# Performance work log

Measured on AMD Instinct MI355X. Metric: run time of the kernel, lower is better.

The kernel has to match this reference:

```python
import jax, jax.numpy as jnp
import numpy as np

# Dim order: [N, K, C, P, Q, R, S]; memory levels: [L0_Registers, L1_Accumulator, L2_Scratchpad, L3_DRAM]
# Tensor types: 0=Input(N,C,P,Q) 1=Weight(K,C,R,S) 2=Output(N,K,P,Q)
DIM_MASK = jnp.array([[1,0,1,1,1,0,0],
                      [0,1,1,0,0,1,1],
                      [1,1,0,1,1,0,0]], dtype=bool)
# reuse dims: Input->K, Weight->N,P,Q, Output->C,R,S
REUSE_MASK = jnp.array([[0,1,0,0,0,0,0],
                        [1,0,0,1,1,0,0],
                        [0,0,1,0,0,1,1]], dtype=bool)

BYTES = 4.0
CLK_MHZ = 1000.0
DRAM_BW_GB_S = 100.0
PE_MAC_EPA_PJ = 0.56
L0_REG_EPA_PJ = 0.18
L1_BASE_EPA_PJ = 0.52
L1_COEFF_PJ_KB = 0.01
L2_BASE_EPA_PJ = 1.2
L2_COEFF_PJ_KB = 0.002
AREA_PER_PE = 0.01
AREA_PER_KB = 0.005

G = 500000  # number of (unfused) layers / fusion groups


def setup_inputs() -> dict:
    key = jax.random.key(0)
    k1, k2 = jax.random.split(key)
    temporal = 1.0 + jax.random.uniform(k1, (G, 7, 4), dtype=jnp.float32)
    spatial = 1.0 + jax.random.uniform(k2, (G, 7, 4), dtype=jnp.float32)
    return {
        "temporal_factors": temporal,
        "spatial_factors": spatial,
        "num_pes": jnp.array([256.0], dtype=jnp.float32),
        "buffer_sizes_kb": jnp.array([1.0, 64.0, 512.0], dtype=jnp.float32),  # L0, L1, L2
    }


def _masked_prod(x, mask):
    # x: [G,7,L], mask: [3,7] -> [G,3,L] product over masked dims
    return jnp.prod(jnp.where(mask[None, :, :, None], x[:, None, :, :], 1.0), axis=2)


def reference(temporal_factors, spatial_factors, num_pes, buffer_sizes_kb):
    pe = num_pes[0]
    sq = jnp.sqrt(pe)

    cumTS = jnp.cumprod(temporal_factors * spatial_factors, axis=2)  # prefix prod over levels
    cumT = jnp.cumprod(temporal_factors, axis=2)
    sufT = jnp.flip(jnp.cumprod(jnp.flip(temporal_factors, 2), 2), 2)  # suffix prod over levels

    macs = jnp.prod(cumTS[:, :, -1], axis=1)  # [G] product of full dim sizes

    fp = _masked_prod(cumTS, DIM_MASK)      # [G,3,4] data footprint up to level l
    outer = _masked_prod(sufT, DIM_MASK)    # [G,3,4] outer iterations from level l up
    ru = _masked_prod(cumT, REUSE_MASK)     # [G,3,4] reuse factor up to level l

    # interfaces (upper->lower): L3->L2, L2->L1, L1->L0
    low = jnp.array([2, 1, 0])
    up = jnp.array([3, 2, 1])
    acc = (fp[:, :, low] * (outer[:, :, up] / (ru[:, :, low] + 1e-9)) * BYTES).sum(axis=1)  # [G,3]

    # latency
    onchip_bw = 2.0 * sq * BYTES * CLK_MHZ * 1e6 / 1e9
    bw = jnp.stack([jnp.full((), DRAM_BW_GB_S), onchip_bw, onchip_bw])  # upper level bw per interface
    mem_lat = acc / (bw[None, :] * 1e9 + 1e-9)
    comp_lat = macs / (pe * CLK_MHZ * 1e6 + 1e-9)
    total_latency = jnp.maximum(comp_lat, mem_lat.max(axis=1)).sum()

    # energy (per interface, keyed by lower level: L2, L1, L0)
    epa = jnp.stack([
        L2_BASE_EPA_PJ + L2_COEFF_PJ_KB * buffer_sizes_kb[2],
        L1_BASE_EPA_PJ + L1_COEFF_PJ_KB * (buffer_sizes_kb[1] / sq),
        jnp.full((), L0_REG_EPA_PJ),
    ])
    total_energy = (macs * PE_MAC_EPA_PJ).sum() + ((acc / 4.0) @ epa).sum()

    # buffer mismatch for buffer levels L0, L1, L2
    req_kb = fp[:, :, :3].sum(axis=1) * BYTES / 1024.0  # [G,3]
    deficit = jax.nn.relu(req_kb - buffer_sizes_kb[None, :])
    total_mismatch = (deficit ** 2).sum()

    area = pe * AREA_PER_PE + (buffer_sizes_kb * AREA_PER_KB).sum()
    return (total_latency, total_energy, area, total_mismatch)
```

## Files before the change

### kernel.cpp

```cpp
#include <hip/hip_runtime.h>
#include <hip/hip_bf16.h>


typedef const __attribute__((address_space(1))) void* gptr_t;
typedef __attribute__((address_space(3))) void* lptr_t;

#define BLK   256
#define NBK   256
#define WPB   4
#define NWAVE (NBK * WPB)
#define TGRP  64

__device__ __forceinline__ float fast_rcp(float x) {
    float r;
    asm("v_rcp_f32 %0, %1" : "=v"(r) : "v"(x));
    return r;
}

__global__ __launch_bounds__(BLK) void hpm_main(
    const float* __restrict__ T, const float* __restrict__ S,
    const float* __restrict__ PE, const float* __restrict__ BUF,
    double* __restrict__ part, int G)
{
    __shared__ float lds[WPB][2][2][TGRP * 28];

    const int tid  = threadIdx.x;
    const int w    = tid >> 6;
    const int lane = tid & 63;
    const int W    = blockIdx.x * WPB + w;
    const int NT   = G / TGRP;
    const int cnt  = (NT > W) ? ((NT - 1 - W) / NWAVE + 1) : 0;

    const float pe = PE[0];
    const float sq = sqrtf(pe);
    const float b0 = BUF[0], b1 = BUF[1], b2 = BUF[2];
    const float inv_bw_dram   = 1.0f / (100.0f * 1e9f + 1e-9f);
    const float inv_bw_onchip = 1.0f / (sq * 8e9f + 1e-9f);
    const float epa0 = 1.2f  + 0.002f * b2;
    const float epa1 = 0.52f + 0.01f  * (b1 / sq);
    const float epa2 = 0.18f;
    const float inv_pe = 1.0f / (pe * 1e9f + 1e-9f);
    asm volatile("s_waitcnt vmcnt(0) lgkmcnt(0)" ::: "memory");

    constexpr unsigned IN_D = 0x1D, WT_D = 0x66, OU_D = 0x1B;
    constexpr unsigned IN_R = 0x02, WT_R = 0x19, OU_R = 0x64;

    auto issue = [&](int t, int buf) {
        const float* gT = T + (size_t)t * (TGRP * 28);
        const float* gS = S + (size_t)t * (TGRP * 28);
        #pragma unroll
        for (int k = 0; k < 7; ++k) {
            const int fo = (k * 64 + lane) * 4;
            __builtin_amdgcn_global_load_lds((gptr_t)(gT + fo),
                                             (lptr_t)&lds[w][buf][0][k * 256], 16, 0, 0);
            __builtin_amdgcn_global_load_lds((gptr_t)(gS + fo),
                                             (lptr_t)&lds[w][buf][1][k * 256], 16, 0, 0);
        }
    };

    double latA = 0.0, enA = 0.0, misA = 0.0;

    auto accumulate = [&](const float4* tv, const float4* sv) {
        float fpI[3] = {1.f,1.f,1.f}, fpW[3] = {1.f,1.f,1.f}, fpO[3] = {1.f,1.f,1.f};
        float otI[3] = {1.f,1.f,1.f}, otW[3] = {1.f,1.f,1.f}, otO[3] = {1.f,1.f,1.f};
        float ruI[3] = {1.f,1.f,1.f}, ruW[3] = {1.f,1.f,1.f}, ruO[3] = {1.f,1.f,1.f};
        float macs = 1.f;

        #pragma unroll
        for (int d = 0; d < 7; ++d) {
            const float4 tt = tv[d];
            const float4 ss = sv[d];

            const float ct0 = tt.x;
            const float ct1 = ct0 * tt.y;
            const float ct2 = ct1 * tt.z;
            const float u0 = tt.x * ss.x, u1 = tt.y * ss.y;
            const float u2 = tt.z * ss.z, u3 = tt.w * ss.w;
            const float cs0 = u0;
            const float cs1 = cs0 * u1;
            const float cs2 = cs1 * u2;
            const float cs3 = cs2 * u3;
            const float st3 = tt.w;
            const float st2 = tt.z * st3;
            const float st1 = tt.y * st2;

            macs *= cs3;

            if ((IN_D >> d) & 1) {
                fpI[0] *= cs0; fpI[1] *= cs1; fpI[2] *= cs2;
                otI[0] *= st1; otI[1] *= st2; otI[2] *= st3;
            }
            if ((WT_D >> d) & 1) {
                fpW[0] *= cs0; fpW[1] *= cs1; fpW[2] *= cs2;
                otW[0] *= st1; otW[1] *= st2; otW[2] *= st3;
            }
            if ((OU_D >> d) & 1) {
                fpO[0] *= cs0; fpO[1] *= cs1; fpO[2] *= cs2;
                otO[0] *= st1; otO[1] *= st2; otO[2] *= st3;
            }
            if ((IN_R >> d) & 1) { ruI[0] *= ct0; ruI[1] *= ct1; ruI[2] *= ct2; }
            if ((WT_R >> d) & 1) { ruW[0] *= ct0; ruW[1] *= ct1; ruW[2] *= ct2; }
            if ((OU_R >> d) & 1) { ruO[0] *= ct0; ruO[1] *= ct1; ruO[2] *= ct2; }
        }

        const float acc0 = 4.f * ( fpI[2] * otI[2] * fast_rcp(ruI[2] + 1e-9f)
                                 + fpW[2] * otW[2] * fast_rcp(ruW[2] + 1e-9f)
                                 + fpO[2] * otO[2] * fast_rcp(ruO[2] + 1e-9f) );
        const float acc1 = 4.f * ( fpI[1] * otI[1] * fast_rcp(ruI[1] + 1e-9f)
                                 + fpW[1] * otW[1] * fast_rcp(ruW[1] + 1e-9f)
                                 + fpO[1] * otO[1] * fast_rcp(ruO[1] + 1e-9f) );
        const float acc2 = 4.f * ( fpI[0] * otI[0] * fast_rcp(ruI[0] + 1e-9f)
                                 + fpW[0] * otW[0] * fast_rcp(ruW[0] + 1e-9f)
                                 + fpO[0] * otO[0] * fast_rcp(ruO[0] + 1e-9f) );

        const float ml = fmaxf(acc0 * inv_bw_dram, fmaxf(acc1, acc2) * inv_bw_onchip);
        const float cl = macs * inv_pe;
        latA += (double)fmaxf(cl, ml);

        enA += (double)(macs * 0.56f + (acc0 * epa0 + acc1 * epa1 + acc2 * epa2) * 0.25f);

        const float c = 4.f / 1024.f;
        const float r0 = (fpI[0] + fpW[0] + fpO[0]) * c;
        const float r1 = (fpI[1] + fpW[1] + fpO[1]) * c;
        const float r2 = (fpI[2] + fpW[2] + fpO[2]) * c;
        const float d0 = fmaxf(r0 - b0, 0.f);
        const float d1 = fmaxf(r1 - b1, 0.f);
        const float d2 = fmaxf(r2 - b2, 0.f);
        misA += (double)d0 * d0 + (double)d1 * d1 + (double)d2 * d2;
    };

    if (cnt > 0) issue(W, 0);
    if (cnt > 1) issue(W + NWAVE, 1);

    for (int i = 0; i < cnt; ++i) {
        if (i + 1 < cnt) asm volatile("s_waitcnt vmcnt(14)" ::: "memory");
        else             asm volatile("s_waitcnt vmcnt(0)"  ::: "memory");

        const int buf = i & 1;
        float4 tv[7], sv[7];
        {
            const float4* Tl = reinterpret_cast<const float4*>(&lds[w][buf][0][lane * 28]);
            const float4* Sl = reinterpret_cast<const float4*>(&lds[w][buf][1][lane * 28]);
            #pragma unroll
            for (int d = 0; d < 7; ++d) { tv[d] = Tl[d]; sv[d] = Sl[d]; }
        }
        asm volatile("s_waitcnt lgkmcnt(0)" ::: "memory");
        __builtin_amdgcn_sched_barrier(0);

        if (i + 2 < cnt) issue(W + (i + 2) * NWAVE, buf);

        accumulate(tv, sv);
    }

    if (W == NWAVE - 1) {
        const int g = NT * TGRP + lane;
        if (g < G) {
            float4 tv[7], sv[7];
            const float4* Tp = reinterpret_cast<const float4*>(T) + (size_t)g * 7;
            const float4* Sp = reinterpret_cast<const float4*>(S) + (size_t)g * 7;
            #pragma unroll
            for (int d = 0; d < 7; ++d) { tv[d] = Tp[d]; sv[d] = Sp[d]; }
            accumulate(tv, sv);
        }
    }

    #pragma unroll
    for (int off = 32; off > 0; off >>= 1) {
        latA += __shfl_down(latA, off);
        enA  += __shfl_down(enA,  off);
        misA += __shfl_down(misA, off);
    }

    __shared__ double sred[3][WPB];
    if (lane == 0) { sred[0][w] = latA; sred[1][w] = enA; sred[2][w] = misA; }
    __syncthreads();

    if (tid == 0) {
        double L = 0.0, E = 0.0, M = 0.0;
        #pragma unroll
        for (int v = 0; v < WPB; ++v) { L += sred[0][v]; E += sred[1][v]; M += sred[2][v]; }
        part[0 * NBK + blockIdx.x] = L;
        part[1 * NBK + blockIdx.x] = E;
        part[2 * NBK + blockIdx.x] = M;
    }
}

__global__ __launch_bounds__(256) void hpm_final(
    const double* __restrict__ part,
    const float* __restrict__ PE, const float* __restrict__ BUF,
    float* __restrict__ out)
{
    const int tid = threadIdx.x;
    double L = 0.0, E = 0.0, M = 0.0;
    if (tid < NBK) {
        L = part[0 * NBK + tid];
        E = part[1 * NBK + tid];
        M = part[2 * NBK + tid];
    }

    #pragma unroll
    for (int off = 32; off > 0; off >>= 1) {
        L += __shfl_down(L, off);
        E += __shfl_down(E, off);
        M += __shfl_down(M, off);
    }

    __shared__ double sred[3][4];
    const int wid  = tid >> 6;
    const int lane = tid & 63;
    if (lane == 0) { sred[0][wid] = L; sred[1][wid] = E; sred[2][wid] = M; }
    __syncthreads();

    if (tid == 0) {
        double Lt = 0.0, Et = 0.0, Mt = 0.0;
        #pragma unroll
        for (int v = 0; v < 4; ++v) { Lt += sred[0][v]; Et += sred[1][v]; Mt += sred[2][v]; }
        out[0] = (float)Lt;
        out[1] = (float)Et;
        out[2] = PE[0] * 0.01f + (BUF[0] + BUF[1] + BUF[2]) * 0.005f;
        out[3] = (float)Mt;
    }
}

extern "C" void kernel_launch(void* const* d_in, const int* in_sizes, int n_in,
                              void* d_out, int out_size, void* d_ws, size_t ws_size,
                              hipStream_t stream) {
    const float* T   = (const float*)d_in[0];
    const float* S   = (const float*)d_in[1];
    const float* PE  = (const float*)d_in[2];
    const float* BUF = (const float*)d_in[3];
    float* out = (float*)d_out;
    double* ws = (double*)d_ws;

    const int G = in_sizes[0] / 28;

    hipLaunchKernelGGL(hpm_main, dim3(NBK), dim3(BLK), 0, stream,
                       T, S, PE, BUF, ws, G);
    hipLaunchKernelGGL(hpm_final, dim3(1), dim3(256), 0, stream,
                       ws, PE, BUF, out);
}
```

Baseline: 25.93 us.

## Replace persistent LDS-pipelined waves with one-thread-per-layer grid and direct loads

Drops the persistent 256-block kernel that double-buffered tiles through LDS with global_load_lds. Each thread now handles one layer, loading its 28 floats straight from global memory with float4 loads, and the grid grows to about 1954 blocks. The final kernel loops over the larger partial array. This removes the async-copy pipeline and its waitcnt management, but gives up the coalesced staging: each thread's 112-byte stride loads are less coalesced, and there are more partials to reduce.

Measured after the change: 27.18 us. 1.05x slower.

```diff
diff --git a/kernel.cpp b/kernel.cpp
--- a/kernel.cpp
+++ b/kernel.cpp
@@ -2,14 +2,7 @@
 #include <hip/hip_bf16.h>
 
 
-typedef const __attribute__((address_space(1))) void* gptr_t;
-typedef __attribute__((address_space(3))) void* lptr_t;
-
-#define BLK   256
-#define NBK   256
-#define WPB   4
-#define NWAVE (NBK * WPB)
-#define TGRP  64
+#define BLK 256
 
 __device__ __forceinline__ float fast_rcp(float x) {
     float r;
@@ -20,51 +13,39 @@
 __global__ __launch_bounds__(BLK) void hpm_main(
     const float* __restrict__ T, const float* __restrict__ S,
     const float* __restrict__ PE, const float* __restrict__ BUF,
-    double* __restrict__ part, int G)
+    double* __restrict__ part, int G, int NB)
 {
-    __shared__ float lds[WPB][2][2][TGRP * 28];
+    const int tid = threadIdx.x;
+    const int g   = blockIdx.x * BLK + tid;
 
-    const int tid  = threadIdx.x;
-    const int w    = tid >> 6;
-    const int lane = tid & 63;
-    const int W    = blockIdx.x * WPB + w;
-    const int NT   = G / TGRP;
-    const int cnt  = (NT > W) ? ((NT - 1 - W) / NWAVE + 1) : 0;
+    double lat = 0.0, en = 0.0, mis = 0.0;
 
-    const float pe = PE[0];
-    const float sq = sqrtf(pe);
-    const float b0 = BUF[0], b1 = BUF[1], b2 = BUF[2];
-    const float inv_bw_dram   = 1.0f / (100.0f * 1e9f + 1e-9f);
-    const float inv_bw_onchip = 1.0f / (sq * 8e9f + 1e-9f);
-    const float epa0 = 1.2f  + 0.002f * b2;
-    const float epa1 = 0.52f + 0.01f  * (b1 / sq);
-    const float epa2 = 0.18f;
-    const float inv_pe = 1.0f / (pe * 1e9f + 1e-9f);
-    asm volatile("s_waitcnt vmcnt(0) lgkmcnt(0)" ::: "memory");
+    if (g < G) {
+        float4 tv[7], sv[7];
+        const float4* Tp = reinterpret_cast<const float4*>(T) + (size_t)g * 7;
+        const float4* Sp = reinterpret_cast<const float4*>(S) + (size_t)g * 7;
+        #pragma unroll
+        for (int d = 0; d < 7; ++d) tv[d] = Tp[d];
+        #pragma unroll
+        for (int d = 0; d < 7; ++d) sv[d] = Sp[d];
 
-    constexpr unsigned IN_D = 0x1D, WT_D = 0x66, OU_D = 0x1B;
-    constexpr unsigned IN_R = 0x02, WT_R = 0x19, OU_R = 0x64;
+        const float pe = PE[0];
+        const float sq = sqrtf(pe);
+        const float b0 = BUF[0], b1 = BUF[1], b2 = BUF[2];
+        const float inv_bw_dram   = 1.0f / (100.0f * 1e9f + 1e-9f);
+        const float inv_bw_onchip = 1.0f / (sq * 8e9f + 1e-9f);
+        const float epa0 = 1.2f  + 0.002f * b2;
+        const float epa1 = 0.52f + 0.01f  * (b1 / sq);
+        const float epa2 = 0.18f;
+        const float inv_pe = 1.0f / (pe * 1e9f + 1e-9f);
 
-    auto issue = [&](int t, int buf) {
-        const float* gT = T + (size_t)t * (TGRP * 28);
-        const float* gS = S + (size_t)t * (TGRP * 28);
-        #pragma unroll
-        for (int k = 0; k < 7; ++k) {
-            const int fo = (k * 64 + lane) * 4;
-            __builtin_amdgcn_global_load_lds((gptr_t)(gT + fo),
-                                             (lptr_t)&lds[w][buf][0][k * 256], 16, 0, 0);
-            __builtin_amdgcn_global_load_lds((gptr_t)(gS + fo),
-                                             (lptr_t)&lds[w][buf][1][k * 256], 16, 0, 0);
-        }
-    };
-
-    double latA = 0.0, enA = 0.0, misA = 0.0;
-
-    auto accumulate = [&](const float4* tv, const float4* sv) {
         float fpI[3] = {1.f,1.f,1.f}, fpW[3] = {1.f,1.f,1.f}, fpO[3] = {1.f,1.f,1.f};
         float otI[3] = {1.f,1.f,1.f}, otW[3] = {1.f,1.f,1.f}, otO[3] = {1.f,1.f,1.f};
         float ruI[3] = {1.f,1.f,1.f}, ruW[3] = {1.f,1.f,1.f}, ruO[3] = {1.f,1.f,1.f};
         float macs = 1.f;
+
+        constexpr unsigned IN_D = 0x1D, WT_D = 0x66, OU_D = 0x1B;
+        constexpr unsigned IN_R = 0x02, WT_R = 0x19, OU_R = 0x64;
 
         #pragma unroll
         for (int d = 0; d < 7; ++d) {
@@ -115,9 +96,9 @@
 
         const float ml = fmaxf(acc0 * inv_bw_dram, fmaxf(acc1, acc2) * inv_bw_onchip);
         const float cl = macs * inv_pe;
-        latA += (double)fmaxf(cl, ml);
+        lat = (double)fmaxf(cl, ml);
 
-        enA += (double)(macs * 0.56f + (acc0 * epa0 + acc1 * epa1 + acc2 * epa2) * 0.25f);
+        en = (double)(macs * 0.56f + (acc0 * epa0 + acc1 * epa1 + acc2 * epa2) * 0.25f);
 
         const float c = 4.f / 1024.f;
         const float r0 = (fpI[0] + fpW[0] + fpO[0]) * c;
@@ -126,76 +107,43 @@
         const float d0 = fmaxf(r0 - b0, 0.f);
         const float d1 = fmaxf(r1 - b1, 0.f);
         const float d2 = fmaxf(r2 - b2, 0.f);
-        misA += (double)d0 * d0 + (double)d1 * d1 + (double)d2 * d2;
-    };
-
-    if (cnt > 0) issue(W, 0);
-    if (cnt > 1) issue(W + NWAVE, 1);
-
-    for (int i = 0; i < cnt; ++i) {
-        if (i + 1 < cnt) asm volatile("s_waitcnt vmcnt(14)" ::: "memory");
-        else             asm volatile("s_waitcnt vmcnt(0)"  ::: "memory");
-
-        const int buf = i & 1;
-        float4 tv[7], sv[7];
-        {
-            const float4* Tl = reinterpret_cast<const float4*>(&lds[w][buf][0][lane * 28]);
-            const float4* Sl = reinterpret_cast<const float4*>(&lds[w][buf][1][lane * 28]);
-            #pragma unroll
-            for (int d = 0; d < 7; ++d) { tv[d] = Tl[d]; sv[d] = Sl[d]; }
-        }
-        asm volatile("s_waitcnt lgkmcnt(0)" ::: "memory");
-        __builtin_amdgcn_sched_barrier(0);
-
-        if (i + 2 < cnt) issue(W + (i + 2) * NWAVE, buf);
-
-        accumulate(tv, sv);
-    }
-
-    if (W == NWAVE - 1) {
-        const int g = NT * TGRP + lane;
-        if (g < G) {
-            float4 tv[7], sv[7];
-            const float4* Tp = reinterpret_cast<const float4*>(T) + (size_t)g * 7;
-            const float4* Sp = reinterpret_cast<const float4*>(S) + (size_t)g * 7;
-            #pragma unroll
-            for (int d = 0; d < 7; ++d) { tv[d] = Tp[d]; sv[d] = Sp[d]; }
-            accumulate(tv, sv);
-        }
+        mis = (double)d0 * d0 + (double)d1 * d1 + (double)d2 * d2;
     }
 
     #pragma unroll
     for (int off = 32; off > 0; off >>= 1) {
-        latA += __shfl_down(latA, off);
-        enA  += __shfl_down(enA,  off);
-        misA += __shfl_down(misA, off);
+        lat += __shfl_down(lat, off);
+        en  += __shfl_down(en,  off);
+        mis += __shfl_down(mis, off);
     }
 
-    __shared__ double sred[3][WPB];
-    if (lane == 0) { sred[0][w] = latA; sred[1][w] = enA; sred[2][w] = misA; }
+    __shared__ double sred[3][4];
+    const int wid  = tid >> 6;
+    const int lane = tid & 63;
+    if (lane == 0) { sred[0][wid] = lat; sred[1][wid] = en; sred[2][wid] = mis; }
     __syncthreads();
 
     if (tid == 0) {
         double L = 0.0, E = 0.0, M = 0.0;
         #pragma unroll
-        for (int v = 0; v < WPB; ++v) { L += sred[0][v]; E += sred[1][v]; M += sred[2][v]; }
-        part[0 * NBK + blockIdx.x] = L;
-        part[1 * NBK + blockIdx.x] = E;
-        part[2 * NBK + blockIdx.x] = M;
+        for (int v = 0; v < 4; ++v) { L += sred[0][v]; E += sred[1][v]; M += sred[2][v]; }
+        part[0 * NB + blockIdx.x] = L;
+        part[1 * NB + blockIdx.x] = E;
+        part[2 * NB + blockIdx.x] = M;
     }
 }
 
 __global__ __launch_bounds__(256) void hpm_final(
-    const double* __restrict__ part,
+    const double* __restrict__ part, int NB,
     const float* __restrict__ PE, const float* __restrict__ BUF,
     float* __restrict__ out)
 {
     const int tid = threadIdx.x;
     double L = 0.0, E = 0.0, M = 0.0;
-    if (tid < NBK) {
-        L = part[0 * NBK + tid];
-        E = part[1 * NBK + tid];
-        M = part[2 * NBK + tid];
+    for (int i = tid; i < NB; i += 256) {
+        L += part[0 * NB + i];
+        E += part[1 * NB + i];
+        M += part[2 * NB + i];
     }
 
     #pragma unroll
@@ -232,10 +180,11 @@
     float* out = (float*)d_out;
     double* ws = (double*)d_ws;
 
-    const int G = in_sizes[0] / 28;
+    const int G  = in_sizes[0] / 28;
+    const int NB = (G + BLK - 1) / BLK;
 
-    hipLaunchKernelGGL(hpm_main, dim3(NBK), dim3(BLK), 0, stream,
-                       T, S, PE, BUF, ws, G);
+    hipLaunchKernelGGL(hpm_main, dim3(NB), dim3(BLK), 0, stream,
+                       T, S, PE, BUF, ws, G, NB);
     hipLaunchKernelGGL(hpm_final, dim3(1), dim3(256), 0, stream,
-                       ws, PE, BUF, out);
+                       ws, NB, PE, BUF, out);
 }
```
